# Performance work log

Measured on AMD Instinct MI355X. Metric: run time of the kernel, lower is better.

The kernel has to match this reference:

```python
import jax, jax.numpy as jnp
import numpy as np

N_U, N_P, E = 200000, 50000, 500000
D_U, D_P, H, OUT = 100, 50, 128, 1
BN_EPS = 1e-5


def _lin(k, dout, din):
    s = 1.0 / np.sqrt(din)
    kw, kb = jax.random.split(k)
    W = jax.random.uniform(kw, (dout, din), jnp.float32, -s, s)
    b = jax.random.uniform(kb, (dout,), jnp.float32, -s, s)
    return W, b


def setup_inputs() -> dict:
    key = jax.random.key(0)
    ks = jax.random.split(key, 12)
    x_u = jax.random.normal(ks[0], (N_U, D_U), jnp.float32)
    x_p = jax.random.normal(ks[1], (N_P, D_P), jnp.float32)
    src = jax.random.randint(ks[2], (E,), 0, N_U, jnp.int64) if jax.config.jax_enable_x64 else jax.random.randint(ks[2], (E,), 0, N_U)
    dst = jax.random.randint(ks[3], (E,), N_U, N_U + N_P)
    edge_index = jnp.stack([src, dst]).astype(jnp.int32)
    W_u, b_u = _lin(ks[4], H, D_U)
    W_p, b_p = _lin(ks[5], H, D_P)
    W1l, b1l = _lin(ks[6], H, H)   # SAGEConv lin_l (aggregated neighbors, carries bias)
    W1r, _ = _lin(ks[7], H, H)     # SAGEConv lin_r (root, no bias)
    W2l, b2l = _lin(ks[8], H, H)
    W2r, _ = _lin(ks[9], H, H)
    W_out, b_out = _lin(ks[10], OUT, H)
    return dict(x_u=x_u, x_p=x_p, edge_index=edge_index,
                W_u=W_u, b_u=b_u, W_p=W_p, b_p=b_p,
                W1l=W1l, b1l=b1l, W1r=W1r,
                g1=jnp.ones((H,), jnp.float32), be1=jnp.zeros((H,), jnp.float32),
                W2l=W2l, b2l=b2l, W2r=W2r,
                g2=jnp.ones((H,), jnp.float32), be2=jnp.zeros((H,), jnp.float32),
                W_out=W_out, b_out=b_out)


def reference(x_u, x_p, edge_index, W_u, b_u, W_p, b_p,
              W1l, b1l, W1r, g1, be1, W2l, b2l, W2r, g2, be2,
              W_out, b_out):
    N = x_u.shape[0] + x_p.shape[0]
    # input projections + relu, then concat users/products -> [N, H]
    x = jnp.concatenate([jax.nn.relu(x_u @ W_u.T + b_u),
                         jax.nn.relu(x_p @ W_p.T + b_p)], axis=0)
    # to_undirected: add reversed edges (bipartite => no duplicates)
    src = jnp.concatenate([edge_index[0], edge_index[1]])
    dst = jnp.concatenate([edge_index[1], edge_index[0]])
    deg = jnp.maximum(jax.ops.segment_sum(jnp.ones_like(dst, jnp.float32), dst, num_segments=N), 1.0)

    def sage(h, Wl, bl, Wr):
        # mean aggregation of neighbor features, scatter by dst
        mean = jax.ops.segment_sum(h[src], dst, num_segments=N) / deg[:, None]
        return mean @ Wl.T + bl + h @ Wr.T

    def bn(h, g, b):
        m = h.mean(0)
        v = h.var(0)  # biased variance, as used for normalization in torch BN
        return (h - m) * jax.lax.rsqrt(v + BN_EPS) * g + b

    h1 = jax.nn.relu(bn(sage(x, W1l, b1l, W1r), g1, be1))   # dropout = identity (eval)
    h2 = jax.nn.relu(bn(sage(h1, W2l, b2l, W2r), g2, be2)) + x
    return h2[: x_u.shape[0]] @ W_out.T + b_out
```

## Files before the change

kernel.cpp:

```cpp
#include <hip/hip_runtime.h>
#include <hip/hip_bf16.h>
#include <cstdint>
#include <cstddef>

#define NT   250000
#define NUU  200000
#define NPP  50000
#define EG   500000
#define E2   1000000
#define HD   128
#define NBLK_SCAN 977

#define CNT2_OFF   0ull
#define SPART2_OFF 1000000ull
#define SS2_OFF    1065536ull
#define RPTR2_OFF  1067584ull
#define BSUM2_OFF  2067588ull
#define BMAT2_OFF  2071504ull
#define COL2_OFF   2251728ull
#define X2_OFF     6251728ull
#define R1B_OFF    70251728ull
#define C2_OFF     134251728ull
#define WS_SPLIT   198251728ull

typedef __hip_bfloat16 bf16;
typedef __attribute__((ext_vector_type(8))) short short8v;
typedef __attribute__((ext_vector_type(4))) float f32x4;

__device__ inline float b2f(short s) { return __builtin_bit_cast(float, ((unsigned)(unsigned short)s) << 16); }
__device__ inline unsigned short f2bf(float f) { return __builtin_bit_cast(unsigned short, __float2bfloat16(f)); }

__global__ __launch_bounds__(256) void k_zero(int* __restrict__ p, int n) {
    for (int i = blockIdx.x * 256 + threadIdx.x; i < n; i += gridDim.x * 256) p[i] = 0;
}

__global__ __launch_bounds__(256) void k_count(const int* __restrict__ ei, int* __restrict__ cnt) {
    for (int e = blockIdx.x * 256 + threadIdx.x; e < E2; e += gridDim.x * 256) {
        int d = (e < EG) ? ei[e + EG] : ei[e - EG];
        atomicAdd(&cnt[d], 1);
    }
}

__global__ __launch_bounds__(256) void k_scan1(const int* __restrict__ cnt, int* __restrict__ bsum) {
    __shared__ int lds[256];
    int i = blockIdx.x * 256 + threadIdx.x;
    int v = (i < NT) ? cnt[i] : 0;
    lds[threadIdx.x] = v; __syncthreads();
    for (int s = 128; s > 0; s >>= 1) {
        if (threadIdx.x < s) lds[threadIdx.x] += lds[threadIdx.x + s];
        __syncthreads();
    }
    if (threadIdx.x == 0) bsum[blockIdx.x] = lds[0];
}

__global__ __launch_bounds__(1024) void k_scan2(int* __restrict__ bsum) {
    __shared__ int lds[1024];
    int i = threadIdx.x;
    int v = (i < NBLK_SCAN) ? bsum[i] : 0;
    lds[i] = v; __syncthreads();
    for (int off = 1; off < 1024; off <<= 1) {
        int t = (i >= off) ? lds[i - off] : 0;
        __syncthreads();
        lds[i] += t;
        __syncthreads();
    }
    if (i < NBLK_SCAN) bsum[i] = lds[i] - v;
}

__global__ __launch_bounds__(256) void k_scan3(const int* __restrict__ cnt, const int* __restrict__ bsum,
                                               int* __restrict__ rp) {
    __shared__ int lds[256];
    int i = blockIdx.x * 256 + threadIdx.x;
    int v = (i < NT) ? cnt[i] : 0;
    lds[threadIdx.x] = v; __syncthreads();
    for (int off = 1; off < 256; off <<= 1) {
        int t = (threadIdx.x >= off) ? lds[threadIdx.x - off] : 0;
        __syncthreads();
        lds[threadIdx.x] += t;
        __syncthreads();
    }
    if (i < NT) rp[i] = bsum[blockIdx.x] + lds[threadIdx.x] - v;
    if (i == 0 && blockIdx.x == 0) rp[NT] = E2;
}

__global__ __launch_bounds__(256) void k_fill(const int* __restrict__ ei, const int* __restrict__ rp,
                                              int* __restrict__ fill, int* __restrict__ col) {
    for (int e = blockIdx.x * 256 + threadIdx.x; e < E2; e += gridDim.x * 256) {
        int s = ei[e];
        int d = (e < EG) ? ei[e + EG] : ei[e - EG];
        int slot = rp[d] + atomicAdd(&fill[d], 1);
        col[slot] = s;
    }
}

__global__ __launch_bounds__(256) void k_wcvt(const float* __restrict__ W1l, const float* __restrict__ W1r,
                                              const float* __restrict__ W2l, const float* __restrict__ W2r,
                                              const float* __restrict__ Wu, const float* __restrict__ Wp,
                                              bf16* __restrict__ B) {
    int i = blockIdx.x * 256 + threadIdx.x;
    if (i < 65536) {
        int layer = i >> 15, rem = i & 32767, o = rem >> 8, k = rem & 255;
        const float* W = layer ? ((k < 128) ? W2l : W2r) : ((k < 128) ? W1l : W1r);
        B[i] = __float2bfloat16(W[o * 128 + (k & 127)]);
    } else if (i < 81920) {
        int rem = i - 65536, o = rem >> 7, k = rem & 127;
        B[i] = __float2bfloat16((k < 100) ? Wu[o * 100 + k] : 0.f);
    } else if (i < 90112) {
        int rem = i - 81920, o = rem >> 6, k = rem & 63;
        B[i] = __float2bfloat16((k < 50) ? Wp[o * 50 + k] : 0.f);
    }
}

template<int DIN, int KPAD>
__global__ __launch_bounds__(256) void k_projm(const float* __restrict__ in, const bf16* __restrict__ Bp,
                                               const float* __restrict__ bias, bf16* __restrict__ outp,
                                               int nrows, int rowbase) {
    const int lane = threadIdx.x & 63;
    const int wid = threadIdx.x >> 6;
    const int wr = wid >> 1, wc = wid & 1;
    const int r15 = lane & 15, l4 = lane >> 4;
    const int tb = blockIdx.x * 128;
    constexpr int NKS = KPAD / 32;

    f32x4 acc[4][4] = {};
#pragma unroll
    for (int ks = 0; ks < NKS; ks++) {
        int kk = ks * 32 + l4 * 8;
        short8v a[4], b[4];
#pragma unroll
        for (int m = 0; m < 4; m++) {
            int r = tb + wr * 64 + m * 16 + r15;
            if (r > nrows - 1) r = nrows - 1;
            const float* src = in + (size_t)r * DIN + kk;
            short8v v;
            if (ks * 32 + 32 <= DIN) {
                if constexpr (DIN % 4 == 0) {
                    const float4* s4 = (const float4*)src;
                    float4 f0 = s4[0], f1 = s4[1];
                    v[0] = (short)f2bf(f0.x); v[1] = (short)f2bf(f0.y);
                    v[2] = (short)f2bf(f0.z); v[3] = (short)f2bf(f0.w);
                    v[4] = (short)f2bf(f1.x); v[5] = (short)f2bf(f1.y);
                    v[6] = (short)f2bf(f1.z); v[7] = (short)f2bf(f1.w);
                } else {
                    const float2* s2 = (const float2*)src;
                    float2 f0 = s2[0], f1 = s2[1], f2 = s2[2], f3 = s2[3];
                    v[0] = (short)f2bf(f0.x); v[1] = (short)f2bf(f0.y);
                    v[2] = (short)f2bf(f1.x); v[3] = (short)f2bf(f1.y);
                    v[4] = (short)f2bf(f2.x); v[5] = (short)f2bf(f2.y);
                    v[6] = (short)f2bf(f3.x); v[7] = (short)f2bf(f3.y);
                }
            } else {
#pragma unroll
                for (int j = 0; j < 8; j++) {
                    float f = (kk + j < DIN) ? src[j] : 0.f;
                    v[j] = (short)f2bf(f);
                }
            }
            a[m] = v;
        }
#pragma unroll
        for (int n = 0; n < 4; n++) {
            int c = wc * 64 + n * 16 + r15;
            b[n] = *(const short8v*)(Bp + (size_t)c * KPAD + kk);
        }
#pragma unroll
        for (int m = 0; m < 4; m++)
#pragma unroll
            for (int n = 0; n < 4; n++)
                acc[m][n] = __builtin_amdgcn_mfma_f32_16x16x32_bf16(a[m], b[n], acc[m][n], 0, 0, 0);
    }
    float bcol[4];
#pragma unroll
    for (int n = 0; n < 4; n++) bcol[n] = bias[wc * 64 + n * 16 + r15];
#pragma unroll
    for (int m = 0; m < 4; m++)
#pragma unroll
        for (int n = 0; n < 4; n++)
#pragma unroll
            for (int g = 0; g < 4; g++) {
                int row = tb + wr * 64 + m * 16 + l4 * 4 + g;
                if (row < nrows) {
                    float v = fmaxf(acc[m][n][g] + bcol[n], 0.f);
                    outp[(size_t)(rowbase + row) * HD + wc * 64 + n * 16 + r15] = __float2bfloat16(v);
                }
            }
}

template<bool NORM>
__global__ __launch_bounds__(256) void k_spmm(const bf16* __restrict__ hin, const float* __restrict__ ssv,
                                              const int* __restrict__ rp, const int* __restrict__ col,
                                              bf16* __restrict__ M) {
    const int tid = threadIdx.x;
    const int gid = tid >> 3, l8 = tid & 7;
    const int fo = l8 * 8;
    float sva[8], tva[8], svb[8], tvb[8];
    if (NORM) {
#pragma unroll
        for (int j = 0; j < 8; j++) {
            sva[j] = ssv[fo + j];      tva[j] = ssv[HD + fo + j];
            svb[j] = ssv[64 + fo + j]; tvb[j] = ssv[HD + 64 + fo + j];
        }
    }
    for (int n = blockIdx.x * 32 + gid; n < NT; n += gridDim.x * 32) {
        int s0 = rp[n], s1 = rp[n + 1];
        float a[8] = {}, b[8] = {};
        for (int p = s0; p < s1; p += 4) {
            int i1 = min(p + 1, s1 - 1), i2 = min(p + 2, s1 - 1), i3 = min(p + 3, s1 - 1);
            int c0 = col[p], c1 = col[i1], c2 = col[i2], c3 = col[i3];
            const bf16* r0p = hin + (size_t)c0 * HD + fo;
            const bf16* r1p = hin + (size_t)c1 * HD + fo;
            const bf16* r2p = hin + (size_t)c2 * HD + fo;
            const bf16* r3p = hin + (size_t)c3 * HD + fo;
            short8v uA0 = *(const short8v*)r0p, uB0 = *(const short8v*)(r0p + 64);
            short8v uA1 = *(const short8v*)r1p, uB1 = *(const short8v*)(r1p + 64);
            short8v uA2 = *(const short8v*)r2p, uB2 = *(const short8v*)(r2p + 64);
            short8v uA3 = *(const short8v*)r3p, uB3 = *(const short8v*)(r3p + 64);
            float m1 = (p + 1 < s1) ? 1.f : 0.f;
            float m2 = (p + 2 < s1) ? 1.f : 0.f;
            float m3 = (p + 3 < s1) ? 1.f : 0.f;
#pragma unroll
            for (int j = 0; j < 8; j++) {
                float vA0 = b2f(uA0[j]), vA1 = b2f(uA1[j]), vA2 = b2f(uA2[j]), vA3 = b2f(uA3[j]);
                float vB0 = b2f(uB0[j]), vB1 = b2f(uB1[j]), vB2 = b2f(uB2[j]), vB3 = b2f(uB3[j]);
                if (NORM) {
                    vA0 = fmaxf(fmaf(vA0, sva[j], tva[j]), 0.f);
                    vA1 = fmaxf(fmaf(vA1, sva[j], tva[j]), 0.f);
                    vA2 = fmaxf(fmaf(vA2, sva[j], tva[j]), 0.f);
                    vA3 = fmaxf(fmaf(vA3, sva[j], tva[j]), 0.f);
                    vB0 = fmaxf(fmaf(vB0, svb[j], tvb[j]), 0.f);
                    vB1 = fmaxf(fmaf(vB1, svb[j], tvb[j]), 0.f);
                    vB2 = fmaxf(fmaf(vB2, svb[j], tvb[j]), 0.f);
                    vB3 = fmaxf(fmaf(vB3, svb[j], tvb[j]), 0.f);
                }
                a[j] += vA0 + m1 * vA1 + m2 * vA2 + m3 * vA3;
                b[j] += vB0 + m1 * vB1 + m2 * vB2 + m3 * vB3;
            }
        }
        float inv = 1.f / (float)max(s1 - s0, 1);
        short8v wa, wb;
#pragma unroll
        for (int j = 0; j < 8; j++) { wa[j] = (short)f2bf(a[j] * inv); wb[j] = (short)f2bf(b[j] * inv); }
        *(short8v*)(M + (size_t)n * HD + fo) = wa;
        *(short8v*)(M + (size_t)n * HD + 64 + fo) = wb;
    }
}

template<bool NORM>
__global__ __launch_bounds__(256) void k_dense(const bf16* __restrict__ Min, const bf16* __restrict__ hin,
                                               const float* __restrict__ ssv,
                                               const bf16* __restrict__ Bmat, const float* __restrict__ blv,
                                               bf16* __restrict__ outp, float* __restrict__ spart,
                                               int store_n) {
    __shared__ __align__(16) char At[65536];
    const int tid = threadIdx.x;
    const int seg = tid & 15, r0 = tid >> 4;
    const int fo = seg * 8;
    const int tb = blockIdx.x * 128;

    float sv[8], tv[8];
    if (NORM) {
#pragma unroll
        for (int j = 0; j < 8; j++) { sv[j] = ssv[fo + j]; tv[j] = ssv[HD + fo + j]; }
    }

#pragma unroll
    for (int it = 0; it < 8; it++) {
        int row = r0 + it * 16;
        int r = tb + row; if (r > NT - 1) r = NT - 1;
        short8v v = *(const short8v*)(Min + (size_t)r * HD + fo);
        *(short8v*)(At + row * 512 + ((seg * 16) ^ ((row & 7) << 4))) = v;
    }
#pragma unroll
    for (int it = 0; it < 8; it++) {
        int row = r0 + it * 16;
        int r = tb + row; if (r > NT - 1) r = NT - 1;
        short8v v = *(const short8v*)(hin + (size_t)r * HD + fo);
        if (NORM) {
#pragma unroll
            for (int j = 0; j < 8; j++) {
                float f = b2f(v[j]);
                v[j] = (short)f2bf(fmaxf(fmaf(f, sv[j], tv[j]), 0.f));
            }
        }
        *(short8v*)(At + row * 512 + (((16 + seg) * 16) ^ ((row & 7) << 4))) = v;
    }
    __syncthreads();

    const int lane = tid & 63, wid = tid >> 6;
    const int wr = wid >> 1, wc = wid & 1;
    const int r15 = lane & 15, l4 = lane >> 4;
    f32x4 acc[4][4] = {};
#pragma unroll
    for (int ks = 0; ks < 8; ks++) {
        short8v a[4], b[4];
#pragma unroll
        for (int m = 0; m < 4; m++) {
            int rl = wr * 64 + m * 16 + r15;
            a[m] = *(const short8v*)(At + rl * 512 + ((ks * 64 + l4 * 16) ^ ((rl & 7) << 4)));
        }
#pragma unroll
        for (int n = 0; n < 4; n++) {
            int c = wc * 64 + n * 16 + r15;
            b[n] = *(const short8v*)(Bmat + (size_t)c * 256 + ks * 32 + l4 * 8);
        }
#pragma unroll
        for (int m = 0; m < 4; m++)
#pragma unroll
            for (int n = 0; n < 4; n++)
                acc[m][n] = __builtin_amdgcn_mfma_f32_16x16x32_bf16(a[m], b[n], acc[m][n], 0, 0, 0);
    }

    float bcol[4];
#pragma unroll
    for (int n = 0; n < 4; n++) bcol[n] = blv[wc * 64 + n * 16 + r15];
    float ls[4] = {0.f, 0.f, 0.f, 0.f}, lq[4] = {0.f, 0.f, 0.f, 0.f};
#pragma unroll
    for (int m = 0; m < 4; m++)
#pragma unroll
        for (int n = 0; n < 4; n++)
#pragma unroll
            for (int gg = 0; gg < 4; gg++) {
                int row = tb + wr * 64 + m * 16 + l4 * 4 + gg;
                float v = acc[m][n][gg] + bcol[n];
                if (row < NT) { ls[n] += v; lq[n] += v * v; }
                if (row < store_n)
                    outp[(size_t)row * HD + wc * 64 + n * 16 + r15] = __float2bfloat16(v);
            }
    int part = (blockIdx.x & 31) * 256;
#pragma unroll
    for (int n = 0; n < 4; n++) {
        float s = ls[n], q2 = lq[n];
        s  += __shfl_xor(s, 16);  s  += __shfl_xor(s, 32);
        q2 += __shfl_xor(q2, 16); q2 += __shfl_xor(q2, 32);
        if (l4 == 0) {
            atomicAdd(&spart[part + wc * 64 + n * 16 + r15], s);
            atomicAdd(&spart[part + 128 + wc * 64 + n * 16 + r15], q2);
        }
    }
}

__global__ void k_fin(const float* __restrict__ sp, const float* __restrict__ g,
                      const float* __restrict__ be, float* __restrict__ ssout) {
    int j = threadIdx.x;
    float m = 0.f, q = 0.f;
    for (int i = 0; i < 32; i++) { m += sp[i * 256 + j]; q += sp[i * 256 + 128 + j]; }
    m *= (1.f / (float)NT);
    q = q * (1.f / (float)NT) - m * m;
    float s = g[j] * rsqrtf(q + 1e-5f);
    ssout[j] = s;
    ssout[HD + j] = be[j] - m * s;
}

__global__ __launch_bounds__(256) void k_out(const bf16* __restrict__ r2, const float* __restrict__ ss,
                                             const bf16* __restrict__ x, const float* __restrict__ wout,
                                             const float* __restrict__ bout, float* __restrict__ outp) {
    int lane = threadIdx.x & 63;
    int wv = (blockIdx.x * blockDim.x + threadIdx.x) >> 6;
    int nwv = (gridDim.x * blockDim.x) >> 6;
    int g16 = lane >> 4, l16 = lane & 15;
    int fo = l16 * 8;
    float s8[8], t8[8], w8[8];
#pragma unroll
    for (int j = 0; j < 8; j++) {
        s8[j] = ss[fo + j]; t8[j] = ss[HD + fo + j]; w8[j] = wout[fo + j];
    }
    float bo = bout[0];
    for (int r0 = wv * 4; r0 < NUU; r0 += nwv * 4) {
        int row = r0 + g16;
        short8v a  = *(const short8v*)(r2 + (size_t)row * HD + fo);
        short8v xx = *(const short8v*)(x  + (size_t)row * HD + fo);
        float acc = 0.f;
#pragma unroll
        for (int j = 0; j < 8; j++) {
            float h = fmaxf(fmaf(b2f(a[j]), s8[j], t8[j]), 0.f) + b2f(xx[j]);
            acc += h * w8[j];
        }
        acc += __shfl_xor(acc, 1);
        acc += __shfl_xor(acc, 2);
        acc += __shfl_xor(acc, 4);
        acc += __shfl_xor(acc, 8);
        if (l16 == 0) outp[row] = acc + bo;
    }
}

extern "C" void kernel_launch(void* const* d_in, const int* in_sizes, int n_in,
                              void* d_out, int out_size, void* d_ws, size_t ws_size,
                              hipStream_t stream) {
    const float* x_u = (const float*)d_in[0];
    const float* x_p = (const float*)d_in[1];
    const int*   ei  = (const int*)d_in[2];
    const float* W_u = (const float*)d_in[3];
    const float* b_u = (const float*)d_in[4];
    const float* W_p = (const float*)d_in[5];
    const float* b_p = (const float*)d_in[6];
    const float* W1l = (const float*)d_in[7];
    const float* b1l = (const float*)d_in[8];
    const float* W1r = (const float*)d_in[9];
    const float* g1  = (const float*)d_in[10];
    const float* be1 = (const float*)d_in[11];
    const float* W2l = (const float*)d_in[12];
    const float* b2l = (const float*)d_in[13];
    const float* W2r = (const float*)d_in[14];
    const float* g2  = (const float*)d_in[15];
    const float* be2 = (const float*)d_in[16];
    const float* Wout = (const float*)d_in[17];
    const float* bout = (const float*)d_in[18];
    float* out = (float*)d_out;
    char* ws = (char*)d_ws;

    if (ws_size < WS_SPLIT) {
        k_zero<<<512, 256, 0, stream>>>((int*)d_out, out_size);
        return;
    }

    int*  cnt    = (int*)(ws + CNT2_OFF);
    float* spart = (float*)(ws + SPART2_OFF);
    float* ssbuf = (float*)(ws + SS2_OFF);
    int*  rp     = (int*)(ws + RPTR2_OFF);
    int*  bsum   = (int*)(ws + BSUM2_OFF);
    bf16* Bmat   = (bf16*)(ws + BMAT2_OFF);
    int*  col    = (int*)(ws + COL2_OFF);
    bf16* X      = (bf16*)(ws + X2_OFF);
    bf16* R1     = (bf16*)(ws + R1B_OFF);
    bf16* MC     = (bf16*)(ws + C2_OFF);

    k_zero<<<1043, 256, 0, stream>>>(cnt, 266896);
    k_wcvt<<<352, 256, 0, stream>>>(W1l, W1r, W2l, W2r, W_u, W_p, Bmat);

    k_count<<<1024, 256, 0, stream>>>(ei, cnt);
    k_scan1<<<NBLK_SCAN, 256, 0, stream>>>(cnt, bsum);
    k_scan2<<<1, 1024, 0, stream>>>(bsum);
    k_scan3<<<NBLK_SCAN, 256, 0, stream>>>(cnt, bsum, rp);
    k_zero<<<977, 256, 0, stream>>>(cnt, NT);
    k_fill<<<1024, 256, 0, stream>>>(ei, rp, cnt, col);

    k_projm<100, 128><<<1563, 256, 0, stream>>>(x_u, Bmat + 65536, b_u, X, NUU, 0);
    k_projm<50, 64><<<391, 256, 0, stream>>>(x_p, Bmat + 81920, b_p, X, NPP, NUU);

    k_spmm<false><<<2048, 256, 0, stream>>>(X, nullptr, rp, col, MC);
    k_dense<false><<<1954, 256, 0, stream>>>(MC, X, nullptr, Bmat, b1l, R1, spart, NT);
    k_fin<<<1, 128, 0, stream>>>(spart, g1, be1, ssbuf);

    k_spmm<true><<<2048, 256, 0, stream>>>(R1, ssbuf, rp, col, MC);
    k_dense<true><<<1954, 256, 0, stream>>>(MC, R1, ssbuf, Bmat + 32768, b2l, MC, spart + 8192, NUU);
    k_fin<<<1, 128, 0, stream>>>(spart + 8192, g2, be2, ssbuf + 256);

    k_out<<<1024, 256, 0, stream>>>(MC, ssbuf + 256, X, Wout, bout, out);
}
```

Baseline: 484.2 us.

## Stage projection inputs through LDS and halve dense-kernel shared memory via two-phase K

The input projection kernel now loads each 128-row fp32 tile once with coalesced float2 reads, converts it to bf16 into a swizzled LDS tile with zeroed K padding, and feeds the MFMAs from LDS. Before, every wave re-read strided global rows per k-step. The dense SAGE kernel splits its 256-wide K into two 128-wide phases that reuse one 32KB LDS buffer: first the aggregated mean, then the root features. This halves shared memory per block, which should allow more blocks per CU, at the cost of an extra barrier and serialized loading between the phases.

```diff
diff --git a/kernel.cpp b/kernel.cpp
--- a/kernel.cpp
+++ b/kernel.cpp
@@ -115,53 +115,47 @@
 __global__ __launch_bounds__(256) void k_projm(const float* __restrict__ in, const bf16* __restrict__ Bp,
                                                const float* __restrict__ bias, bf16* __restrict__ outp,
                                                int nrows, int rowbase) {
-    const int lane = threadIdx.x & 63;
-    const int wid = threadIdx.x >> 6;
+    __shared__ __align__(16) char As[128 * KPAD * 2];
+    const int tid = threadIdx.x;
+    const int tb = blockIdx.x * 128;
+    constexpr int RSTRIDE = KPAD * 2;
+    constexpr int PADE = KPAD - DIN;
+    constexpr int PH = PADE / 2;
+    constexpr int PPAD = 128 * PH;
+    constexpr int PMAIN = 128 * DIN / 2;
+
+    for (int q = tid; q < PPAD; q += 256) {
+        int row = q / PH;
+        int k = DIN + (q - row * PH) * 2;
+        *(unsigned*)(As + row * RSTRIDE + ((((k >> 3) << 4) ^ ((row & 7) << 4)) + (k & 7) * 2)) = 0u;
+    }
+    for (int q = tid; q < PMAIN; q += 256) {
+        int f = q * 2;
+        int row = f / DIN, k = f - row * DIN;
+        int rg = tb + row; if (rg > nrows - 1) rg = nrows - 1;
+        float2 v = *(const float2*)(in + (size_t)rg * DIN + k);
+        unsigned u = (unsigned)f2bf(v.x) | ((unsigned)f2bf(v.y) << 16);
+        *(unsigned*)(As + row * RSTRIDE + ((((k >> 3) << 4) ^ ((row & 7) << 4)) + (k & 7) * 2)) = u;
+    }
+    __syncthreads();
+
+    const int lane = tid & 63, wid = tid >> 6;
     const int wr = wid >> 1, wc = wid & 1;
     const int r15 = lane & 15, l4 = lane >> 4;
-    const int tb = blockIdx.x * 128;
     constexpr int NKS = KPAD / 32;
-
     f32x4 acc[4][4] = {};
 #pragma unroll
     for (int ks = 0; ks < NKS; ks++) {
-        int kk = ks * 32 + l4 * 8;
         short8v a[4], b[4];
 #pragma unroll
         for (int m = 0; m < 4; m++) {
-            int r = tb + wr * 64 + m * 16 + r15;
-            if (r > nrows - 1) r = nrows - 1;
-            const float* src = in + (size_t)r * DIN + kk;
-            short8v v;
-            if (ks * 32 + 32 <= DIN) {
-                if constexpr (DIN % 4 == 0) {
-                    const float4* s4 = (const float4*)src;
-                    float4 f0 = s4[0], f1 = s4[1];
-                    v[0] = (short)f2bf(f0.x); v[1] = (short)f2bf(f0.y);
-                    v[2] = (short)f2bf(f0.z); v[3] = (short)f2bf(f0.w);
-                    v[4] = (short)f2bf(f1.x); v[5] = (short)f2bf(f1.y);
-                    v[6] = (short)f2bf(f1.z); v[7] = (short)f2bf(f1.w);
-                } else {
-                    const float2* s2 = (const float2*)src;
-                    float2 f0 = s2[0], f1 = s2[1], f2 = s2[2], f3 = s2[3];
-                    v[0] = (short)f2bf(f0.x); v[1] = (short)f2bf(f0.y);
-                    v[2] = (short)f2bf(f1.x); v[3] = (short)f2bf(f1.y);
-                    v[4] = (short)f2bf(f2.x); v[5] = (short)f2bf(f2.y);
-                    v[6] = (short)f2bf(f3.x); v[7] = (short)f2bf(f3.y);
-                }
-            } else {
-#pragma unroll
-                for (int j = 0; j < 8; j++) {
-                    float f = (kk + j < DIN) ? src[j] : 0.f;
-                    v[j] = (short)f2bf(f);
-                }
-            }
-            a[m] = v;
+            int rl = wr * 64 + m * 16 + r15;
+            a[m] = *(const short8v*)(As + rl * RSTRIDE + ((ks * 64 + l4 * 16) ^ ((rl & 7) << 4)));
         }
 #pragma unroll
         for (int n = 0; n < 4; n++) {
             int c = wc * 64 + n * 16 + r15;
-            b[n] = *(const short8v*)(Bp + (size_t)c * KPAD + kk);
+            b[n] = *(const short8v*)(Bp + (size_t)c * KPAD + ks * 32 + l4 * 8);
         }
 #pragma unroll
         for (int m = 0; m < 4; m++)
@@ -251,7 +245,7 @@
                                                const bf16* __restrict__ Bmat, const float* __restrict__ blv,
                                                bf16* __restrict__ outp, float* __restrict__ spart,
                                                int store_n) {
-    __shared__ __align__(16) char At[65536];
+    __shared__ __align__(16) char At[32768];
     const int tid = threadIdx.x;
     const int seg = tid & 15, r0 = tid >> 4;
     const int fo = seg * 8;
@@ -263,13 +257,40 @@
         for (int j = 0; j < 8; j++) { sv[j] = ssv[fo + j]; tv[j] = ssv[HD + fo + j]; }
     }
 
+    const int lane = tid & 63, wid = tid >> 6;
+    const int wr = wid >> 1, wc = wid & 1;
+    const int r15 = lane & 15, l4 = lane >> 4;
+    f32x4 acc[4][4] = {};
+
 #pragma unroll
     for (int it = 0; it < 8; it++) {
         int row = r0 + it * 16;
         int r = tb + row; if (r > NT - 1) r = NT - 1;
         short8v v = *(const short8v*)(Min + (size_t)r * HD + fo);
-        *(short8v*)(At + row * 512 + ((seg * 16) ^ ((row & 7) << 4))) = v;
-    }
+        *(short8v*)(At + row * 256 + ((seg * 16) ^ ((row & 7) << 4))) = v;
+    }
+    __syncthreads();
+#pragma unroll
+    for (int ks = 0; ks < 4; ks++) {
+        short8v a[4], b[4];
+#pragma unroll
+        for (int m = 0; m < 4; m++) {
+            int rl = wr * 64 + m * 16 + r15;
+            a[m] = *(const short8v*)(At + rl * 256 + ((ks * 64 + l4 * 16) ^ ((rl & 7) << 4)));
+        }
+#pragma unroll
+        for (int n = 0; n < 4; n++) {
+            int c = wc * 64 + n * 16 + r15;
+            b[n] = *(const short8v*)(Bmat + (size_t)c * 256 + ks * 32 + l4 * 8);
+        }
+#pragma unroll
+        for (int m = 0; m < 4; m++)
+#pragma unroll
+            for (int n = 0; n < 4; n++)
+                acc[m][n] = __builtin_amdgcn_mfma_f32_16x16x32_bf16(a[m], b[n], acc[m][n], 0, 0, 0);
+    }
+    __syncthreads();
+
 #pragma unroll
     for (int it = 0; it < 8; it++) {
         int row = r0 + it * 16;
@@ -282,26 +303,21 @@
                 v[j] = (short)f2bf(fmaxf(fmaf(f, sv[j], tv[j]), 0.f));
             }
         }
-        *(short8v*)(At + row * 512 + (((16 + seg) * 16) ^ ((row & 7) << 4))) = v;
+        *(short8v*)(At + row * 256 + ((seg * 16) ^ ((row & 7) << 4))) = v;
     }
     __syncthreads();
-
-    const int lane = tid & 63, wid = tid >> 6;
-    const int wr = wid >> 1, wc = wid & 1;
-    const int r15 = lane & 15, l4 = lane >> 4;
-    f32x4 acc[4][4] = {};
-#pragma unroll
-    for (int ks = 0; ks < 8; ks++) {
+#pragma unroll
+    for (int ks = 0; ks < 4; ks++) {
         short8v a[4], b[4];
 #pragma unroll
         for (int m = 0; m < 4; m++) {
             int rl = wr * 64 + m * 16 + r15;
-            a[m] = *(const short8v*)(At + rl * 512 + ((ks * 64 + l4 * 16) ^ ((rl & 7) << 4)));
+            a[m] = *(const short8v*)(At + rl * 256 + ((ks * 64 + l4 * 16) ^ ((rl & 7) << 4)));
         }
 #pragma unroll
         for (int n = 0; n < 4; n++) {
             int c = wc * 64 + n * 16 + r15;
-            b[n] = *(const short8v*)(Bmat + (size_t)c * 256 + ks * 32 + l4 * 8);
+            b[n] = *(const short8v*)(Bmat + (size_t)c * 256 + (ks + 4) * 32 + l4 * 8);
         }
 #pragma unroll
         for (int m = 0; m < 4; m++)
```

New measurement: 472.6 us. -2.4%, faster.
